# Optimization experiments

Hardware: AMD Instinct MI355X
Metric: run time of the kernel (lower is better)

## Reference

```python
import jax, jax.numpy as jnp
import numpy as np

N_NODES = 100000
N_EDGES = 1600000
C_IN = 128
C_OUT = 128


def setup_inputs() -> dict:
    key = jax.random.key(0)
    k1, k2, k3 = jax.random.split(key, 3)
    x = jax.random.normal(k1, (N_NODES, C_IN), dtype=jnp.float32)
    edge_index = jax.random.randint(k2, (2, N_EDGES), 0, N_NODES, dtype=jnp.int64)
    # Linear(in, out, bias=False) weight has shape [out, in]
    W = jax.random.normal(k3, (C_OUT, C_IN), dtype=jnp.float32) * 0.05
    return {"x": x, "edge_index": edge_index, "W": W}


def reference(x, edge_index, W):
    # Original builds dense A (adj[src,dst] += 1 per edge, counting duplicates),
    # adds self-loops I, computes d = A.sum(dim=0) (column sums = in-degree + 1),
    # then out = diag(1/d) @ A @ diag(1/d) @ (x @ W.T).
    # Equivalent edge-wise O(E) form:
    #   out[i] = (1/d[i]) * ( sum_{(i,j) in edges} h[j]/d[j]  +  h[i]/d[i] )
    N = x.shape[0]
    src, dst = edge_index[0], edge_index[1]
    # d[j] = (# edges with dst=j) + 1 (self-loop)
    deg = jax.ops.segment_sum(jnp.ones(src.shape[0], dtype=x.dtype), dst, num_segments=N) + 1.0
    h = x @ W.T                      # [N, C_out]
    hn = h / deg[:, None]            # h[j]/d[j]
    agg = jax.ops.segment_sum(hn[dst], src, num_segments=N) + hn  # neighbor msgs + self-loop
    return agg / deg[:, None]
```

## Files before the change

### kernel.cpp

```cpp
#include <hip/hip_runtime.h>
#include <hip/hip_bf16.h>

#define C 128
#define TPB 256
#define TPB3 1024
#define BWID 512
#define NBUK 256

typedef __attribute__((ext_vector_type(8))) _Float16 half8;
typedef __attribute__((ext_vector_type(4))) float f32x4;
typedef __attribute__((ext_vector_type(2))) float fv2;
typedef unsigned long long u64;

#define OFF_BSS   0x400
#define OFF_BSD   0xC00
#define OFF_CSUM  0x1400
#define OFF_HISTS 0x10000
#define OFF_HISTD 0x50000
#define OFF_OFFS  0xA0000
#define OFF_CNTS  0x110000
#define OFF_INVD  0x180000
#define OFF_EDST  0x200000
#define OFF_HN    0x900000

__device__ __forceinline__ unsigned f2bf_bits(float f) {
    unsigned u = __float_as_uint(f);
    return (u + 0x7fffu + ((u >> 16) & 1u)) >> 16;
}

__global__ __launch_bounds__(TPB3) void hist_kernel(const void* __restrict__ edges,
                                                    long long E, int chunk,
                                                    int* __restrict__ src32,
                                                    int* __restrict__ dst32,
                                                    int* __restrict__ histS,
                                                    int* __restrict__ histD) {
    __shared__ int flag_s;
    __shared__ int hs[NBUK], hd[NBUK];
    const int t = threadIdx.x;
    const int B = blockIdx.x;
    if (t == 0) flag_s = 0;
    if (t < NBUK) { hs[t] = 0; hd[t] = 0; }
    __syncthreads();
    {
        const unsigned* ew = (const unsigned*)edges;
        int any = 0;
        for (int k = t; k < 2048; k += TPB3) {
            const long long widx = 2LL * k + 1;
            if (widx < 2 * E) any |= (ew[widx] != 0u);
        }
        if (any) atomicOr(&flag_s, 1);
    }
    __syncthreads();
    const int is32 = flag_s;
    const long long b0 = (long long)B * chunk;
    for (int i = t; i < chunk; i += TPB3) {
        const long long e = b0 + i;
        if (e < E) {
            int s, d;
            if (is32) {
                const int* p = (const int*)edges;
                s = p[e]; d = p[E + e];
            } else {
                const long long* p = (const long long*)edges;
                s = (int)p[e]; d = (int)p[E + e];
            }
            src32[e] = s;
            dst32[e] = d;
            atomicAdd(&hs[s >> 9], 1);
            atomicAdd(&hd[d >> 9], 1);
        }
    }
    __syncthreads();
    if (t < NBUK) {
        histS[B * NBUK + t] = hs[t];
        histD[B * NBUK + t] = hd[t];
    }
}

__global__ __launch_bounds__(TPB) void colscan_kernel(int* __restrict__ histS,
                                                      int* __restrict__ histD,
                                                      int* __restrict__ csum) {
    __shared__ int s[TPB];
    const int t = threadIdx.x;
    const int which = blockIdx.x >> 8;
    const int b = blockIdx.x & (NBUK - 1);
    int* hist = which ? histD : histS;
    const int v = hist[t * NBUK + b];
    s[t] = v;
    __syncthreads();
    for (int d = 1; d < TPB; d <<= 1) {
        const int a = (t >= d) ? s[t - d] : 0;
        __syncthreads();
        s[t] += a;
        __syncthreads();
    }
    hist[t * NBUK + b] = s[t] - v;
    if (t == TPB - 1) csum[which * NBUK + b] = s[t];
}

__global__ __launch_bounds__(TPB) void bscan_kernel(const int* __restrict__ csum,
                                                    int* __restrict__ bsS,
                                                    int* __restrict__ bsD, int Etot) {
    __shared__ int s[TPB];
    const int t = threadIdx.x;
    int v = csum[t];
    s[t] = v;
    __syncthreads();
    for (int d = 1; d < TPB; d <<= 1) {
        const int a = (t >= d) ? s[t - d] : 0;
        __syncthreads();
        s[t] += a;
        __syncthreads();
    }
    bsS[t] = s[t] - v;
    if (t == TPB - 1) bsS[NBUK] = Etot;
    __syncthreads();
    v = csum[NBUK + t];
    s[t] = v;
    __syncthreads();
    for (int d = 1; d < TPB; d <<= 1) {
        const int a = (t >= d) ? s[t - d] : 0;
        __syncthreads();
        s[t] += a;
        __syncthreads();
    }
    bsD[t] = s[t] - v;
    if (t == TPB - 1) bsD[NBUK] = Etot;
}

__global__ __launch_bounds__(TPB3) void scatter_kernel(const int* __restrict__ src32,
                                                       const int* __restrict__ dst32,
                                                       long long E, int chunk,
                                                       const int* __restrict__ histS,
                                                       const int* __restrict__ histD,
                                                       const int* __restrict__ bsS,
                                                       const int* __restrict__ bsD,
                                                       u64* __restrict__ partS,
                                                       int* __restrict__ partD) {
    __shared__ int cs[NBUK], cd[NBUK];
    const int t = threadIdx.x;
    const int B = blockIdx.x;
    if (t < NBUK) {
        cs[t] = histS[B * NBUK + t] + bsS[t];
        cd[t] = histD[B * NBUK + t] + bsD[t];
    }
    __syncthreads();
    const long long b0 = (long long)B * chunk;
    for (int i = t; i < chunk; i += TPB3) {
        const long long e = b0 + i;
        if (e < E) {
            const int sv = src32[e], dv = dst32[e];
            const int ps = atomicAdd(&cs[sv >> 9], 1);
            partS[ps] = ((u64)(unsigned)dv << 32) | (unsigned)sv;
            const int pd = atomicAdd(&cd[dv >> 9], 1);
            partD[pd] = dv;
        }
    }
}

__global__ __launch_bounds__(TPB3) void csrdeg_kernel(const u64* __restrict__ partS,
                                                      const int* __restrict__ partD,
                                                      const int* __restrict__ bsS,
                                                      const int* __restrict__ bsD,
                                                      int* __restrict__ offS,
                                                      int* __restrict__ cntS,
                                                      int* __restrict__ eDst,
                                                      float* __restrict__ invd, int N) {
    __shared__ int cnt[BWID], off[BWID], s[TPB3];
    const int t = threadIdx.x;
    const int B = blockIdx.x;
    const int lo = B * BWID;
    if (lo >= N) return;
    const int eb = bsS[B], ee = bsS[B + 1];
    if (t < BWID) cnt[t] = 0;
    __syncthreads();
    for (int e = eb + t; e < ee; e += TPB3)
        atomicAdd(&cnt[(int)(partS[e] & 0xffffffffu) - lo], 1);
    __syncthreads();
    const int loc = (t < BWID) ? cnt[t] : 0;
    s[t] = loc;
    __syncthreads();
    for (int d = 1; d < TPB3; d <<= 1) {
        const int a = (t >= d) ? s[t - d] : 0;
        __syncthreads();
        s[t] += a;
        __syncthreads();
    }
    const int ex = s[t] - loc;
    if (t < BWID) {
        off[t] = ex;
        const int node = lo + t;
        if (node < N) { offS[node] = eb + ex; cntS[node] = loc; }
    }
    __syncthreads();
    for (int e = eb + t; e < ee; e += TPB3) {
        const u64 p = partS[e];
        const int sv = (int)(p & 0xffffffffu);
        const int dv = (int)(p >> 32);
        const int pos = atomicAdd(&off[sv - lo], 1);
        eDst[eb + pos] = dv;
    }
    __syncthreads();
    if (t < BWID) cnt[t] = 0;
    __syncthreads();
    const int db = bsD[B], de = bsD[B + 1];
    for (int e = db + t; e < de; e += TPB3)
        atomicAdd(&cnt[partD[e] - lo], 1);
    __syncthreads();
    if (t < BWID) {
        const int node = lo + t;
        if (node < N) invd[node] = 1.0f / (float)(cnt[t] + 1);
    }
}

__global__ __launch_bounds__(TPB) void gemm_mfma_kernel(const float* __restrict__ x,
                                                        const float* __restrict__ W,
                                                        const float* __restrict__ invd,
                                                        unsigned short* __restrict__ hn,
                                                        int N) {
    __shared__ _Float16 Wl[C * C];
    const int t = threadIdx.x;
    const int lane = t & 63;
    const int wid = t >> 6;
    const int lr = lane & 15;
    const int lk = lane >> 4;
    const int m0 = blockIdx.x * 128 + wid * 32;

    {
        const float4* W4 = (const float4*)W;
#pragma unroll
        for (int i = 0; i < 16; ++i) {
            const int g = i * TPB + t;
            const float4 v = W4[g];
            const int row = g >> 5;
            const int c4 = g & 31;
            const int chunk = c4 >> 1;
            const int half = c4 & 1;
            union { _Float16 h[4]; unsigned long long u; } p;
            p.h[0] = (_Float16)v.x; p.h[1] = (_Float16)v.y;
            p.h[2] = (_Float16)v.z; p.h[3] = (_Float16)v.w;
            const int off = row * 256 + ((chunk ^ (row & 7)) << 4) + (half << 3);
            *(unsigned long long*)((char*)Wl + off) = p.u;
        }
    }

    half8 a[2][4];
#pragma unroll
    for (int mb = 0; mb < 2; ++mb) {
        const int row = m0 + mb * 16 + lr;
        const float* xp = x + (size_t)row * C + lk * 8;
#pragma unroll
        for (int ks = 0; ks < 4; ++ks) {
            half8 av;
            if (row < N) {
                const float4 v0 = *(const float4*)(xp + ks * 32);
                const float4 v1 = *(const float4*)(xp + ks * 32 + 4);
                av[0] = (_Float16)v0.x; av[1] = (_Float16)v0.y;
                av[2] = (_Float16)v0.z; av[3] = (_Float16)v0.w;
                av[4] = (_Float16)v1.x; av[5] = (_Float16)v1.y;
                av[6] = (_Float16)v1.z; av[7] = (_Float16)v1.w;
            } else {
                av = (half8)((_Float16)0.f);
            }
            a[mb][ks] = av;
        }
    }
    __syncthreads();

    f32x4 acc[2][8];
#pragma unroll
    for (int mb = 0; mb < 2; ++mb)
#pragma unroll
        for (int nf = 0; nf < 8; ++nf)
            acc[mb][nf] = (f32x4){0.f, 0.f, 0.f, 0.f};

#pragma unroll
    for (int nf = 0; nf < 8; ++nf) {
        const int brow = nf * 16 + lr;
        half8 b[4];
#pragma unroll
        for (int ks = 0; ks < 4; ++ks) {
            const int chunkp = (lk + ks * 4) ^ (lr & 7);
            b[ks] = *(const half8*)((const char*)Wl + brow * 256 + chunkp * 16);
        }
#pragma unroll
        for (int mb = 0; mb < 2; ++mb)
#pragma unroll
            for (int ks = 0; ks < 4; ++ks)
                acc[mb][nf] = __builtin_amdgcn_mfma_f32_16x16x32_f16(
                    a[mb][ks], b[ks], acc[mb][nf], 0, 0, 0);
    }

#pragma unroll
    for (int mb = 0; mb < 2; ++mb) {
#pragma unroll
        for (int r = 0; r < 4; ++r) {
            const int row = m0 + mb * 16 + lk * 4 + r;
            if (row < N) {
                const float idv = invd[row];
                unsigned short* hp = hn + (size_t)row * C + lr;
#pragma unroll
                for (int nf = 0; nf < 8; ++nf)
                    hp[nf * 16] = (unsigned short)f2bf_bits(acc[mb][nf][r] * idv);
            }
        }
    }
}

__global__ __launch_bounds__(TPB) void gather_kernel(const int* __restrict__ offS,
                                                     const int* __restrict__ cntS,
                                                     const int* __restrict__ eDst,
                                                     const uint4* __restrict__ hnb4,
                                                     const float* __restrict__ invd,
                                                     float* __restrict__ out, int N) {
    const int lane = threadIdx.x & 63;
    const int w = (blockIdx.x * TPB + threadIdx.x) >> 6;
    if (w >= N) return;
    const int sub = lane >> 4;
    const int ll  = lane & 15;
    const int beg = offS[w];
    const int cnt = cntS[w];
    const int total = cnt + 1;

    float acc[8];
#pragma unroll
    for (int i = 0; i < 8; ++i) acc[i] = 0.f;

    for (int j0 = 0; j0 < total; j0 += 64) {
        const int m = min(64, total - j0);
        int dl = w;
        if (lane < m && j0 + lane < cnt)
            dl = __builtin_nontemporal_load(&eDst[beg + j0 + lane]);
#pragma unroll 4
        for (int q = 0; q < m; q += 4) {
            const int d = __shfl(dl, q + sub);
            if (q + sub < m) {
                const uint4 v = hnb4[(size_t)d * 16 + ll];
                acc[0] += __uint_as_float(v.x << 16);
                acc[1] += __uint_as_float(v.x & 0xffff0000u);
                acc[2] += __uint_as_float(v.y << 16);
                acc[3] += __uint_as_float(v.y & 0xffff0000u);
                acc[4] += __uint_as_float(v.z << 16);
                acc[5] += __uint_as_float(v.z & 0xffff0000u);
                acc[6] += __uint_as_float(v.w << 16);
                acc[7] += __uint_as_float(v.w & 0xffff0000u);
            }
        }
    }

#pragma unroll
    for (int i = 0; i < 8; ++i) {
        acc[i] += __shfl_xor(acc[i], 16);
        acc[i] += __shfl_xor(acc[i], 32);
    }

    const float s = invd[w];
    fv2 o;
    o.x = acc[sub * 2] * s;
    o.y = acc[sub * 2 + 1] * s;
    fv2* op = (fv2*)(out + (size_t)w * C + ll * 8 + sub * 2);
    __builtin_nontemporal_store(o, op);
}

extern "C" void kernel_launch(void* const* d_in, const int* in_sizes, int n_in,
                              void* d_out, int out_size, void* d_ws, size_t ws_size,
                              hipStream_t stream) {
    const float* x = (const float*)d_in[0];
    const void* edges = d_in[1];
    const float* W = (const float*)d_in[2];
    float* out = (float*)d_out;

    const int N = in_sizes[0] / C;
    const long long E = (long long)in_sizes[1] / 2;

    char* ws = (char*)d_ws;
    int*       bsS   = (int*)(ws + OFF_BSS);
    int*       bsD   = (int*)(ws + OFF_BSD);
    int*       csum  = (int*)(ws + OFF_CSUM);
    int*       histS = (int*)(ws + OFF_HISTS);
    int*       histD = (int*)(ws + OFF_HISTD);
    int*       offS  = (int*)(ws + OFF_OFFS);
    int*       cntS  = (int*)(ws + OFF_CNTS);
    float*     invd  = (float*)(ws + OFF_INVD);
    int*       eDst  = (int*)(ws + OFF_EDST);
    unsigned short* hn = (unsigned short*)(ws + OFF_HN);

    int* o32   = (int*)d_out;
    int* src32 = o32;
    int* dst32 = o32 + E;
    u64* partS = (u64*)(o32 + 2 * E);
    int* partD = o32 + 6 * E;

    const int chunk = (int)((E + NBUK - 1) / NBUK);

    hist_kernel<<<NBUK, TPB3, 0, stream>>>(edges, E, chunk, src32, dst32,
                                           histS, histD);
    colscan_kernel<<<2 * NBUK, TPB, 0, stream>>>(histS, histD, csum);
    bscan_kernel<<<1, TPB, 0, stream>>>(csum, bsS, bsD, (int)E);
    scatter_kernel<<<NBUK, TPB3, 0, stream>>>(src32, dst32, E, chunk, histS, histD,
                                              bsS, bsD, partS, partD);
    csrdeg_kernel<<<NBUK, TPB3, 0, stream>>>(partS, partD, bsS, bsD,
                                             offS, cntS, eDst, invd, N);

    const int nBlkG = (N + 127) / 128;
    gemm_mfma_kernel<<<nBlkG, TPB, 0, stream>>>(x, W, invd, hn, N);

    const int nBlkA = (N * 64 + TPB - 1) / TPB;
    gather_kernel<<<nBlkA, TPB, 0, stream>>>(offS, cntS, eDst, (const uint4*)hn,
                                             invd, out, N);
}
```

Measured before the change: 141.5 us.

## Vectorize edge loads, skip int32 staging copy, use wave-shuffle scan in CSR build

The histogram and scatter kernels now handle two edges per thread with 2-wide vector loads and stores. When the edge indices are already int32, the hist kernel no longer writes src32/dst32 and scatter reads the original edges directly, selected by a flag stored in the workspace. The csrdeg block prefix scan over 1024 threads is replaced by a wave-level shuffle scan plus a small cross-wave pass, removing many __syncthreads rounds. This adds branching and another global flag read, and the staging skip does not apply to the int64 inputs used by the test.

Measured after the change: 137.8 us. -2.6%, faster.

```diff
diff --git a/kernel.cpp b/kernel.cpp
--- a/kernel.cpp
+++ b/kernel.cpp
@@ -10,8 +10,11 @@
 typedef __attribute__((ext_vector_type(8))) _Float16 half8;
 typedef __attribute__((ext_vector_type(4))) float f32x4;
 typedef __attribute__((ext_vector_type(2))) float fv2;
+typedef __attribute__((ext_vector_type(2))) int iv2;
+typedef __attribute__((ext_vector_type(2))) long long ll2;
 typedef unsigned long long u64;
 
+#define OFF_FLAG  0x0
 #define OFF_BSS   0x400
 #define OFF_BSD   0xC00
 #define OFF_CSUM  0x1400
@@ -33,7 +36,8 @@
                                                     int* __restrict__ src32,
                                                     int* __restrict__ dst32,
                                                     int* __restrict__ histS,
-                                                    int* __restrict__ histD) {
+                                                    int* __restrict__ histD,
+                                                    int* __restrict__ flagp) {
     __shared__ int flag_s;
     __shared__ int hs[NBUK], hd[NBUK];
     const int t = threadIdx.x;
@@ -52,23 +56,44 @@
     }
     __syncthreads();
     const int is32 = flag_s;
+    if (t == 0) *flagp = is32;
+    const int Eeven = ((E & 1) == 0);
     const long long b0 = (long long)B * chunk;
-    for (int i = t; i < chunk; i += TPB3) {
-        const long long e = b0 + i;
-        if (e < E) {
-            int s, d;
-            if (is32) {
-                const int* p = (const int*)edges;
-                s = p[e]; d = p[E + e];
+    for (int i = 2 * t; i < chunk; i += 2 * TPB3) {
+        const long long e0 = b0 + i;
+        const bool v0 = (e0 < E);
+        const bool v1 = (i + 1 < chunk) && (e0 + 1 < E);
+        int s0 = 0, d0 = 0, s1 = 0, d1 = 0;
+        if (is32) {
+            const int* p = (const int*)edges;
+            if (v0 && v1 && Eeven) {
+                const iv2 sv = *(const iv2*)(p + e0);
+                const iv2 dv = *(const iv2*)(p + E + e0);
+                s0 = sv.x; s1 = sv.y; d0 = dv.x; d1 = dv.y;
             } else {
-                const long long* p = (const long long*)edges;
-                s = (int)p[e]; d = (int)p[E + e];
-            }
-            src32[e] = s;
-            dst32[e] = d;
-            atomicAdd(&hs[s >> 9], 1);
-            atomicAdd(&hd[d >> 9], 1);
-        }
+                if (v0) { s0 = p[e0]; d0 = p[E + e0]; }
+                if (v1) { s1 = p[e0 + 1]; d1 = p[E + e0 + 1]; }
+            }
+        } else {
+            const long long* p = (const long long*)edges;
+            if (v0 && v1 && Eeven) {
+                const ll2 sv = *(const ll2*)(p + e0);
+                const ll2 dv = *(const ll2*)(p + E + e0);
+                s0 = (int)sv.x; s1 = (int)sv.y; d0 = (int)dv.x; d1 = (int)dv.y;
+            } else {
+                if (v0) { s0 = (int)p[e0]; d0 = (int)p[E + e0]; }
+                if (v1) { s1 = (int)p[e0 + 1]; d1 = (int)p[E + e0 + 1]; }
+            }
+            if (v0 && v1) {
+                *(iv2*)(src32 + e0) = (iv2){s0, s1};
+                *(iv2*)(dst32 + e0) = (iv2){d0, d1};
+            } else {
+                if (v0) { src32[e0] = s0; dst32[e0] = d0; }
+                if (v1) { src32[e0 + 1] = s1; dst32[e0 + 1] = d1; }
+            }
+        }
+        if (v0) { atomicAdd(&hs[s0 >> 9], 1); atomicAdd(&hd[d0 >> 9], 1); }
+        if (v1) { atomicAdd(&hs[s1 >> 9], 1); atomicAdd(&hd[d1 >> 9], 1); }
     }
     __syncthreads();
     if (t < NBUK) {
@@ -128,7 +153,9 @@
     if (t == TPB - 1) bsD[NBUK] = Etot;
 }
 
-__global__ __launch_bounds__(TPB3) void scatter_kernel(const int* __restrict__ src32,
+__global__ __launch_bounds__(TPB3) void scatter_kernel(const void* __restrict__ edges,
+                                                       const int* __restrict__ flagp,
+                                                       const int* __restrict__ src32,
                                                        const int* __restrict__ dst32,
                                                        long long E, int chunk,
                                                        const int* __restrict__ histS,
@@ -145,15 +172,35 @@
         cd[t] = histD[B * NBUK + t] + bsD[t];
     }
     __syncthreads();
+    const int is32 = *flagp;
+    const int* sp = is32 ? (const int*)edges : src32;
+    const int* dp = is32 ? (const int*)edges + E : dst32;
+    const int Eeven = ((E & 1) == 0);
     const long long b0 = (long long)B * chunk;
-    for (int i = t; i < chunk; i += TPB3) {
-        const long long e = b0 + i;
-        if (e < E) {
-            const int sv = src32[e], dv = dst32[e];
-            const int ps = atomicAdd(&cs[sv >> 9], 1);
-            partS[ps] = ((u64)(unsigned)dv << 32) | (unsigned)sv;
-            const int pd = atomicAdd(&cd[dv >> 9], 1);
-            partD[pd] = dv;
+    for (int i = 2 * t; i < chunk; i += 2 * TPB3) {
+        const long long e0 = b0 + i;
+        const bool v0 = (e0 < E);
+        const bool v1 = (i + 1 < chunk) && (e0 + 1 < E);
+        int s0 = 0, d0 = 0, s1 = 0, d1 = 0;
+        if (v0 && v1 && Eeven) {
+            const iv2 sv = *(const iv2*)(sp + e0);
+            const iv2 dv = *(const iv2*)(dp + e0);
+            s0 = sv.x; s1 = sv.y; d0 = dv.x; d1 = dv.y;
+        } else {
+            if (v0) { s0 = sp[e0]; d0 = dp[e0]; }
+            if (v1) { s1 = sp[e0 + 1]; d1 = dp[e0 + 1]; }
+        }
+        if (v0) {
+            const int ps = atomicAdd(&cs[s0 >> 9], 1);
+            partS[ps] = ((u64)(unsigned)d0 << 32) | (unsigned)s0;
+            const int pd = atomicAdd(&cd[d0 >> 9], 1);
+            partD[pd] = d0;
+        }
+        if (v1) {
+            const int ps = atomicAdd(&cs[s1 >> 9], 1);
+            partS[ps] = ((u64)(unsigned)d1 << 32) | (unsigned)s1;
+            const int pd = atomicAdd(&cd[d1 >> 9], 1);
+            partD[pd] = d1;
         }
     }
 }
@@ -166,11 +213,13 @@
                                                       int* __restrict__ cntS,
                                                       int* __restrict__ eDst,
                                                       float* __restrict__ invd, int N) {
-    __shared__ int cnt[BWID], off[BWID], s[TPB3];
+    __shared__ int cnt[BWID], off[BWID];
+    __shared__ int wtot[16];
     const int t = threadIdx.x;
     const int B = blockIdx.x;
     const int lo = B * BWID;
     if (lo >= N) return;
+    const int wv = t >> 6, ln = t & 63;
     const int eb = bsS[B], ee = bsS[B + 1];
     if (t < BWID) cnt[t] = 0;
     __syncthreads();
@@ -178,15 +227,26 @@
         atomicAdd(&cnt[(int)(partS[e] & 0xffffffffu) - lo], 1);
     __syncthreads();
     const int loc = (t < BWID) ? cnt[t] : 0;
-    s[t] = loc;
-    __syncthreads();
-    for (int d = 1; d < TPB3; d <<= 1) {
-        const int a = (t >= d) ? s[t - d] : 0;
-        __syncthreads();
-        s[t] += a;
-        __syncthreads();
-    }
-    const int ex = s[t] - loc;
+    int v = loc;
+#pragma unroll
+    for (int d = 1; d < 64; d <<= 1) {
+        const int n = __shfl_up(v, d);
+        if (ln >= d) v += n;
+    }
+    if (ln == 63) wtot[wv] = v;
+    __syncthreads();
+    if (wv == 0) {
+        const int wv_ = (ln < 16) ? wtot[ln] : 0;
+        int w2 = wv_;
+#pragma unroll
+        for (int d = 1; d < 16; d <<= 1) {
+            const int n = __shfl_up(w2, d);
+            if (ln >= d) w2 += n;
+        }
+        if (ln < 16) wtot[ln] = w2 - wv_;
+    }
+    __syncthreads();
+    const int ex = v - loc + wtot[wv];
     if (t < BWID) {
         off[t] = ex;
         const int node = lo + t;
@@ -374,6 +434,7 @@
     const long long E = (long long)in_sizes[1] / 2;
 
     char* ws = (char*)d_ws;
+    int*       flagp = (int*)(ws + OFF_FLAG);
     int*       bsS   = (int*)(ws + OFF_BSS);
     int*       bsD   = (int*)(ws + OFF_BSD);
     int*       csum  = (int*)(ws + OFF_CSUM);
@@ -394,11 +455,11 @@
     const int chunk = (int)((E + NBUK - 1) / NBUK);
 
     hist_kernel<<<NBUK, TPB3, 0, stream>>>(edges, E, chunk, src32, dst32,
-                                           histS, histD);
+                                           histS, histD, flagp);
     colscan_kernel<<<2 * NBUK, TPB, 0, stream>>>(histS, histD, csum);
     bscan_kernel<<<1, TPB, 0, stream>>>(csum, bsS, bsD, (int)E);
-    scatter_kernel<<<NBUK, TPB3, 0, stream>>>(src32, dst32, E, chunk, histS, histD,
-                                              bsS, bsD, partS, partD);
+    scatter_kernel<<<NBUK, TPB3, 0, stream>>>(edges, flagp, src32, dst32, E, chunk,
+                                              histS, histD, bsS, bsD, partS, partD);
     csrdeg_kernel<<<NBUK, TPB3, 0, stream>>>(partS, partD, bsS, bsD,
                                              offS, cntS, eDst, invd, N);
 
```
